# Optimization experiments

Measured on AMD Instinct MI355X. Metric: run time of the kernel, lower is better.

Reference implementation:

```python
import jax, jax.numpy as jnp
import numpy as np

B, Q, C = 8, 100, 1024
H, W = 64, 64
NH = 16
HD = C // NH
SCALE = HD ** -0.5
LN_EPS = 1e-5


def setup_inputs() -> dict:
    key = jax.random.key(0)
    ks = jax.random.split(key, 8)
    xav = lambda k, shp: jax.random.normal(k, shp, jnp.float32) * (2.0 / (shp[0] + shp[-1])) ** 0.5
    return {
        "tgt": jax.random.normal(ks[0], (B, Q, C), jnp.float32),
        "memory": jax.random.normal(ks[1], (B, H, W, C), jnp.float32),
        "memory_pos_emb": jax.random.normal(ks[2], (B, H, W, C), jnp.float32),
        "query_pos_emb": jax.random.normal(ks[3], (B, Q, C), jnp.float32),
        "Wq": xav(ks[4], (C, C)),
        "Wk": xav(ks[5], (C, C)),
        "Wv": xav(ks[6], (C, C)),
        "Wo": xav(ks[7], (C, C)),
        "bo": jnp.zeros((C,), jnp.float32),
        "ln_gamma": jnp.ones((C,), jnp.float32),
        "ln_beta": jnp.zeros((C,), jnp.float32),
    }


def _layernorm(x, g, b):
    mu = jnp.mean(x, axis=-1, keepdims=True)
    var = jnp.var(x, axis=-1, keepdims=True)
    return (x - mu) * jax.lax.rsqrt(var + LN_EPS) * g + b


def reference(tgt, memory, memory_pos_emb, query_pos_emb, Wq, Wk, Wv, Wo, bo, ln_gamma, ln_beta):
    # flatten spatial dims: [B,H,W,C] -> [B,K,C]
    mem = memory.reshape(B, H * W, C)
    mpos = memory_pos_emb.reshape(B, H * W, C)
    q_in = tgt + query_pos_emb          # [B,Q,C]
    k_in = mem + mpos                    # [B,K,C]
    # projections (torch Linear: x @ W.T), split heads -> [B,nh,*,hd]
    q = (q_in @ Wq.T).reshape(B, Q, NH, HD).transpose(0, 2, 1, 3)
    k = (k_in @ Wk.T).reshape(B, -1, NH, HD).transpose(0, 2, 1, 3)
    v = (mem @ Wv.T).reshape(B, -1, NH, HD).transpose(0, 2, 1, 3)
    dots = jnp.einsum('bhid,bhjd->bhij', q, k) * SCALE   # [B,nh,Q,K]
    # slot attention: softmax over QUERY axis, then renormalize over keys
    attn = jax.nn.softmax(dots, axis=2)
    attn = attn / (jnp.sum(attn, axis=-1, keepdims=True) + 1e-8)
    updates = jnp.einsum('bhij,bhjd->bhid', attn, v)     # [B,nh,Q,hd]
    updates = updates.transpose(0, 2, 1, 3).reshape(B, Q, C)
    out = updates @ Wo.T + bo
    # residual (dropout is identity in eval) + post-LayerNorm
    return _layernorm(tgt + out, ln_gamma, ln_beta)
```

## Files before the change

kernel.cpp:

```cpp
#include <hip/hip_runtime.h>

typedef unsigned short u16;
typedef __attribute__((ext_vector_type(8))) short bf16x8;
typedef __attribute__((ext_vector_type(4))) short bf16x4;
typedef __attribute__((ext_vector_type(4))) float f32x4;
typedef __attribute__((ext_vector_type(4))) unsigned short u16x4;
typedef __attribute__((ext_vector_type(4))) int i32x4;
typedef __attribute__((ext_vector_type(4))) float f4;

#define DI __device__ __forceinline__


DI u16 f2bf(float f){
  unsigned int u = __float_as_uint(f);
  return (u16)((u + 0x7FFFu + ((u >> 16) & 1u)) >> 16);
}

DI void gl_lds16(const void* g, void* l){
  __builtin_amdgcn_global_load_lds((const __attribute__((address_space(1))) unsigned int*)g,
                                   (__attribute__((address_space(3))) unsigned int*)l, 16, 0, 0);
}

__global__ __launch_bounds__(256) void prep_kv(const float* __restrict__ mem,
                                               const float* __restrict__ mpos,
                                               u16* __restrict__ kA, u16* __restrict__ vA){
  size_t gid = (size_t)blockIdx.x * 256 + threadIdx.x;
  f4 m = ((const f4*)mem)[gid];
  f4 p = ((const f4*)mpos)[gid];
  u16x4 k, v;
  #pragma unroll
  for (int j = 0; j < 4; ++j){ k[j] = f2bf(m[j] + p[j]); v[j] = f2bf(m[j]); }
  ((u16x4*)kA)[gid] = k;
  ((u16x4*)vA)[gid] = v;
}

__global__ __launch_bounds__(256) void prep_qw(const float* __restrict__ tgt,
                                               const float* __restrict__ qpos,
                                               const float* __restrict__ Wq, const float* __restrict__ Wk,
                                               const float* __restrict__ Wv, const float* __restrict__ Wo,
                                               u16* __restrict__ qA, u16* __restrict__ Wbf){
  int gid = blockIdx.x * 256 + threadIdx.x;
  const int NQ4 = 819200 / 4;
  if (gid < NQ4){
    f4 a = ((const f4*)tgt)[gid];
    f4 b = ((const f4*)qpos)[gid];
    u16x4 r;
    #pragma unroll
    for (int j = 0; j < 4; ++j) r[j] = f2bf(a[j] + b[j]);
    ((u16x4*)qA)[gid] = r;
  } else {
    int wid = gid - NQ4;
    int sel = wid >> 18;
    int off = wid & 262143;
    const float* W = (sel == 0) ? Wq : (sel == 1) ? Wk : (sel == 2) ? Wv : Wo;
    f4 w = ((const f4*)W)[off];
    u16x4 r;
    #pragma unroll
    for (int j = 0; j < 4; ++j) r[j] = f2bf(w[j]);
    ((u16x4*)(Wbf))[(size_t)sel * 262144 + off] = r;
  }
}

template<int MODE>
__global__ __launch_bounds__(256, 2) void gemm_bt(
    const u16* __restrict__ A, const u16* __restrict__ Bw,
    u16* __restrict__ Cb, float* __restrict__ Cf,
    const float* __restrict__ bias, const float* __restrict__ resid,
    int M, float scale)
{
  __shared__ u16 lA[2][128 * 32];
  __shared__ u16 lB[2][128 * 32];
  const int tid = threadIdx.x;
  const int l = tid & 63, w = tid >> 6;
  const int nwg = gridDim.x;
  int bid = blockIdx.x;
  bid = (bid & 7) * (nwg >> 3) + (bid >> 3);
  const int mb = bid >> 3, nb = bid & 7;
  const int m0 = mb * 128, n0 = nb * 128;
  const int fr = l & 15, fg = l >> 4;
  const int wr = w >> 1, wc = w & 1;

  f32x4 acc[4][4] = {};

  auto stage = [&](int buf, int kt){
    const int k0 = kt * 32;
    #pragma unroll
    for (int q = 0; q < 2; ++q){
      int r = w * 32 + q * 16 + (l >> 2);
      int ar = m0 + r; if (ar >= M) ar = M - 1;
      gl_lds16(A  + (size_t)ar * 1024 + k0 + (l & 3) * 8, &lA[buf][(w * 32 + q * 16) * 32]);
      gl_lds16(Bw + (size_t)(n0 + r) * 1024 + k0 + (l & 3) * 8, &lB[buf][(w * 32 + q * 16) * 32]);
    }
  };

  stage(0, 0);
  __syncthreads();
  for (int kt = 0; kt < 32; ++kt){
    const int cur = kt & 1;
    if (kt < 31) stage(cur ^ 1, kt + 1);
    bf16x8 av[4], bv[4];
    #pragma unroll
    for (int m = 0; m < 4; ++m)
      av[m] = *(const bf16x8*)&lA[cur][(wr * 64 + m * 16 + fr) * 32 + fg * 8];
    #pragma unroll
    for (int n = 0; n < 4; ++n)
      bv[n] = *(const bf16x8*)&lB[cur][(wc * 64 + n * 16 + fr) * 32 + fg * 8];
    #pragma unroll
    for (int m = 0; m < 4; ++m)
      #pragma unroll
      for (int n = 0; n < 4; ++n)
        acc[m][n] = __builtin_amdgcn_mfma_f32_16x16x32_bf16(av[m], bv[n], acc[m][n], 0, 0, 0);
    __syncthreads();
  }

  #pragma unroll
  for (int m = 0; m < 4; ++m){
    const int grow_base = m0 + wr * 64 + m * 16 + fg * 4;
    #pragma unroll
    for (int n = 0; n < 4; ++n){
      const int gcol = n0 + wc * 64 + n * 16 + fr;
      #pragma unroll
      for (int r = 0; r < 4; ++r){
        const int grow = grow_base + r;
        if (grow < M){
          const float v = acc[m][n][r];
          if (MODE == 0) Cb[(size_t)grow * 1024 + gcol] = f2bf(v * scale);
          else           Cf[(size_t)grow * 1024 + gcol] = v + bias[gcol] + resid[(size_t)grow * 1024 + gcol];
        }
      }
    }
  }
}

__global__ __launch_bounds__(64, 1) void attn_k(
    const u16* __restrict__ qp, const u16* __restrict__ kp, const u16* __restrict__ vp,
    float* __restrict__ updpart, float* __restrict__ rspart)
{
  const int bidx = blockIdx.x;
  const int c = bidx & 7, h = (bidx >> 3) & 15, b = bidx >> 7;
  const int bh = b * 16 + h;
  const int l = threadIdx.x;
  const int fr = l & 15, fg = l >> 4;

  __shared__ u16 qlds[112 * 64];
  for (int t = 0; t < 14; ++t){
    int chunk = t * 64 + l;
    int row = chunk >> 3, cb = chunk & 7;
    i32x4 val = {0, 0, 0, 0};
    if (row < 100)
      val = *(const i32x4*)(qp + (size_t)(b * 100 + row) * 1024 + h * 64 + cb * 8);
    *(i32x4*)((char*)qlds + row * 128 + ((cb ^ (row & 7)) * 16)) = val;
  }
  __syncthreads();

  bf16x8 qf[7][2];
  #pragma unroll
  for (int n = 0; n < 7; ++n)
    #pragma unroll
    for (int ks = 0; ks < 2; ++ks){
      int row = n * 16 + fr;
      int cb = ks * 4 + fg;
      qf[n][ks] = *(const bf16x8*)((const char*)qlds + row * 128 + ((cb ^ (row & 7)) * 16));
    }

  f32x4 acc[7][4] = {};
  float rs[7] = {};
  const f32x4 fz = {0.f, 0.f, 0.f, 0.f};
  const size_t kvbase = ((size_t)b * 4096) * 1024 + h * 64;

  for (int t = 0; t < 32; ++t){
    const int j0 = c * 512 + t * 16;
    bf16x8 kf0 = *(const bf16x8*)(kp + kvbase + (size_t)(j0 + fr) * 1024 + fg * 8);
    bf16x8 kf1 = *(const bf16x8*)(kp + kvbase + (size_t)(j0 + fr) * 1024 + 32 + fg * 8);
    f32x4 s[7];
    #pragma unroll
    for (int n = 0; n < 7; ++n){
      s[n] = __builtin_amdgcn_mfma_f32_16x16x32_bf16(kf0, qf[n][0], fz, 0, 0, 0);
      s[n] = __builtin_amdgcn_mfma_f32_16x16x32_bf16(kf1, qf[n][1], s[n], 0, 0, 0);
    }
    if (fr >= 4){ s[6][0] = -1e30f; s[6][1] = -1e30f; s[6][2] = -1e30f; s[6][3] = -1e30f; }

    float pv[7][4];
    #pragma unroll
    for (int r = 0; r < 4; ++r){
      float m = s[0][r];
      #pragma unroll
      for (int n = 1; n < 7; ++n) m = fmaxf(m, s[n][r]);
      m = fmaxf(m, __shfl_xor(m, 1)); m = fmaxf(m, __shfl_xor(m, 2));
      m = fmaxf(m, __shfl_xor(m, 4)); m = fmaxf(m, __shfl_xor(m, 8));
      float sum = 0.f;
      #pragma unroll
      for (int n = 0; n < 7; ++n){ float e = __expf(s[n][r] - m); pv[n][r] = e; sum += e; }
      sum += __shfl_xor(sum, 1); sum += __shfl_xor(sum, 2);
      sum += __shfl_xor(sum, 4); sum += __shfl_xor(sum, 8);
      float inv = 1.0f / sum;
      #pragma unroll
      for (int n = 0; n < 7; ++n) pv[n][r] *= inv;
    }

    bf16x4 pk[7];
    #pragma unroll
    for (int n = 0; n < 7; ++n){
      rs[n] += pv[n][0] + pv[n][1] + pv[n][2] + pv[n][3];
      bf16x4 t4;
      t4[0] = (short)f2bf(pv[n][0]); t4[1] = (short)f2bf(pv[n][1]);
      t4[2] = (short)f2bf(pv[n][2]); t4[3] = (short)f2bf(pv[n][3]);
      pk[n] = t4;
    }

    bf16x4 vf[4];
    #pragma unroll
    for (int dt = 0; dt < 4; ++dt){
      bf16x4 tv;
      #pragma unroll
      for (int jj = 0; jj < 4; ++jj)
        tv[jj] = (short)vp[kvbase + (size_t)(j0 + fg * 4 + jj) * 1024 + dt * 16 + fr];
      vf[dt] = tv;
    }

    #pragma unroll
    for (int n = 0; n < 7; ++n)
      #pragma unroll
      for (int dt = 0; dt < 4; ++dt)
        acc[n][dt] = __builtin_amdgcn_mfma_f32_16x16x16bf16_1k(vf[dt], pk[n], acc[n][dt], 0, 0, 0);
  }

  #pragma unroll
  for (int n = 0; n < 7; ++n){
    float v = rs[n];
    v += __shfl_xor(v, 16); v += __shfl_xor(v, 32);
    if (l < 16) rspart[((size_t)c * 128 + bh) * 112 + n * 16 + l] = v;
  }
  float* ub = updpart + ((size_t)c * 128 + bh) * 64 * 112;
  #pragma unroll
  for (int n = 0; n < 7; ++n)
    #pragma unroll
    for (int dt = 0; dt < 4; ++dt)
      #pragma unroll
      for (int r = 0; r < 4; ++r){
        int d = dt * 16 + fg * 4 + r;
        int i = n * 16 + fr;
        ub[d * 112 + i] = acc[n][dt][r];
      }
}

__global__ __launch_bounds__(256) void nrm_k(const float* __restrict__ updpart,
                                             const float* __restrict__ rspart,
                                             u16* __restrict__ updn){
  int gid = blockIdx.x * 256 + threadIdx.x;
  int b = gid / 102400;
  int rem = gid % 102400;
  int i = rem / 1024;
  int cc = rem & 1023;
  int h = cc >> 6, d = cc & 63;
  int bh = b * 16 + h;
  float sum = 0.f, rsum = 0.f;
  #pragma unroll
  for (int c = 0; c < 8; ++c){
    sum  += updpart[(((size_t)c * 128 + bh) * 64 + d) * 112 + i];
    rsum += rspart[((size_t)c * 128 + bh) * 112 + i];
  }
  updn[gid] = f2bf(sum / (rsum + 1e-8f));
}

__global__ __launch_bounds__(256) void ln_k(const float* __restrict__ x,
                                            const float* __restrict__ g,
                                            const float* __restrict__ be,
                                            float* __restrict__ out){
  const int row = blockIdx.x;
  const int tid = threadIdx.x;
  const f4 xv = *(const f4*)(x + (size_t)row * 1024 + tid * 4);
  float s = xv[0] + xv[1] + xv[2] + xv[3];
  float q = xv[0]*xv[0] + xv[1]*xv[1] + xv[2]*xv[2] + xv[3]*xv[3];
  #pragma unroll
  for (int m = 1; m < 64; m <<= 1){ s += __shfl_xor(s, m); q += __shfl_xor(q, m); }
  __shared__ float ss[4], qq[4];
  const int w = tid >> 6;
  if ((tid & 63) == 0){ ss[w] = s; qq[w] = q; }
  __syncthreads();
  s = ss[0] + ss[1] + ss[2] + ss[3];
  q = qq[0] + qq[1] + qq[2] + qq[3];
  const float mu = s * (1.0f / 1024.0f);
  const float var = q * (1.0f / 1024.0f) - mu * mu;
  const float rstd = rsqrtf(var + 1e-5f);
  const f4 gv = *(const f4*)(g + tid * 4);
  const f4 bv = *(const f4*)(be + tid * 4);
  f4 o;
  #pragma unroll
  for (int j = 0; j < 4; ++j) o[j] = (xv[j] - mu) * rstd * gv[j] + bv[j];
  *(f4*)(out + (size_t)row * 1024 + tid * 4) = o;
}

extern "C" void kernel_launch(void* const* d_in, const int* in_sizes, int n_in,
                              void* d_out, int out_size, void* d_ws, size_t ws_size,
                              hipStream_t stream)
{
  const float* tgt   = (const float*)d_in[0];
  const float* mem   = (const float*)d_in[1];
  const float* mpos  = (const float*)d_in[2];
  const float* qpos  = (const float*)d_in[3];
  const float* Wq    = (const float*)d_in[4];
  const float* Wk    = (const float*)d_in[5];
  const float* Wv    = (const float*)d_in[6];
  const float* Wo    = (const float*)d_in[7];
  const float* bo    = (const float*)d_in[8];
  const float* gamma = (const float*)d_in[9];
  const float* beta  = (const float*)d_in[10];

  char* ws = (char*)d_ws;
  u16* qA     = (u16*)(ws + 0);
  u16* Wbf    = (u16*)(ws + 1638400);
  u16* kA     = (u16*)(ws + 10027008);
  u16* vA     = (u16*)(ws + 77135872);
  u16* qproj  = (u16*)(ws + 144244736);
  u16* kproj  = (u16*)(ws + 145883136);
  u16* vproj  = kA;
  float* updpart = (float*)(ws + 77135872);
  float* rspart  = (float*)(ws + 77135872 + 29360128);
  u16*   updn    = (u16*)  (ws + 77135872 + 29818880);
  float* resid   = (float*)(ws + 77135872 + 31457280);

  prep_kv<<<32768, 256, 0, stream>>>(mem, mpos, kA, vA);
  prep_qw<<<4896, 256, 0, stream>>>(tgt, qpos, Wq, Wk, Wv, Wo, qA, Wbf);
  gemm_bt<0><<<56,   256, 0, stream>>>(qA, Wbf,            qproj, nullptr, nullptr, nullptr, 800,   0.125f);
  gemm_bt<0><<<2048, 256, 0, stream>>>(kA, Wbf + 1048576,  kproj, nullptr, nullptr, nullptr, 32768, 1.0f);
  gemm_bt<0><<<2048, 256, 0, stream>>>(vA, Wbf + 2097152,  vproj, nullptr, nullptr, nullptr, 32768, 1.0f);
  attn_k<<<1024, 64, 0, stream>>>(qproj, kproj, vproj, updpart, rspart);
  nrm_k<<<3200, 256, 0, stream>>>(updpart, rspart, updn);
  gemm_bt<1><<<56, 256, 0, stream>>>(updn, Wbf + 3145728, nullptr, resid, bo, tgt, 800, 1.0f);
  ln_k<<<800, 256, 0, stream>>>(resid, gamma, beta, (float*)d_out);
}
```

Measured before the change: 415.8 us.

## Add 256x256-tile 8-wave GEMM for K/V projections and batch prep_kv loads

Adds a new gemm256 kernel with 256x256 output tiles, 512 threads, double-buffered LDS staging through global_load_lds, XOR-swizzled LDS reads, and interleaved barriers with setprio around MFMA groups. The large K and V projections now use it in place of the 128-tile gemm_bt, which should raise data reuse per tile and overlap loads with MFMA. Separately, prep_kv now has each thread handle four strided vectors so more loads are in flight per thread. The bigger tile brings high register pressure (128 accumulator floats per thread) and only one block per CU.

```diff
diff --git a/kernel.cpp b/kernel.cpp
--- a/kernel.cpp
+++ b/kernel.cpp
@@ -24,14 +24,24 @@
 __global__ __launch_bounds__(256) void prep_kv(const float* __restrict__ mem,
                                                const float* __restrict__ mpos,
                                                u16* __restrict__ kA, u16* __restrict__ vA){
-  size_t gid = (size_t)blockIdx.x * 256 + threadIdx.x;
-  f4 m = ((const f4*)mem)[gid];
-  f4 p = ((const f4*)mpos)[gid];
-  u16x4 k, v;
-  #pragma unroll
-  for (int j = 0; j < 4; ++j){ k[j] = f2bf(m[j] + p[j]); v[j] = f2bf(m[j]); }
-  ((u16x4*)kA)[gid] = k;
-  ((u16x4*)vA)[gid] = v;
+  const int t = blockIdx.x * 256 + threadIdx.x;
+  const int S = 2097152;
+  f4 m[4], p[4];
+  #pragma unroll
+  for (int i = 0; i < 4; ++i){
+    size_t gid = (size_t)t + (size_t)i * S;
+    m[i] = ((const f4*)mem)[gid];
+    p[i] = ((const f4*)mpos)[gid];
+  }
+  #pragma unroll
+  for (int i = 0; i < 4; ++i){
+    size_t gid = (size_t)t + (size_t)i * S;
+    u16x4 k, v;
+    #pragma unroll
+    for (int j = 0; j < 4; ++j){ k[j] = f2bf(m[i][j] + p[i][j]); v[j] = f2bf(m[i][j]); }
+    ((u16x4*)kA)[gid] = k;
+    ((u16x4*)vA)[gid] = v;
+  }
 }
 
 __global__ __launch_bounds__(256) void prep_qw(const float* __restrict__ tgt,
@@ -58,6 +68,127 @@
     #pragma unroll
     for (int j = 0; j < 4; ++j) r[j] = f2bf(w[j]);
     ((u16x4*)(Wbf))[(size_t)sel * 262144 + off] = r;
+  }
+}
+
+__global__ __launch_bounds__(512, 1) void gemm256(
+    const u16* __restrict__ A, const u16* __restrict__ Bw,
+    u16* __restrict__ Cb, float scale)
+{
+  __shared__ __align__(16) char lds[2][2][2][16384];
+  const int tid = threadIdx.x;
+  const int l = tid & 63, w = tid >> 6;
+  const int nwg = gridDim.x;
+  const int sbid = (blockIdx.x & 7) * (nwg >> 3) + (blockIdx.x >> 3);
+  const int mb = sbid >> 2, nb = sbid & 3;
+  const int m0 = mb * 256, n0 = nb * 256;
+  const int fr = l & 15, fg = l >> 4;
+  const int wm = w >> 2, wn = w & 3;
+
+  const int src_c2 = (l & 3) ^ ((l >> 2) & 3) ^ ((l >> 4) & 3);
+  const int rc16 = ((fg ^ ((fr & 3) ^ ((fr >> 2) & 3))) * 16);
+
+  auto stageAB = [&](int buf, int kt, int kh){
+    #pragma unroll
+    for (int q = 0; q < 2; ++q){
+      const int rr = (q * 8 + w) * 16 + (l >> 2);
+      const size_t gofs = (size_t)kt * 64 + (size_t)kh * 32 + (size_t)src_c2 * 8;
+      gl_lds16(A  + (size_t)(m0 + rr) * 1024 + gofs, &lds[buf][0][kh][(q * 8 + w) * 1024]);
+      gl_lds16(Bw + (size_t)(n0 + rr) * 1024 + gofs, &lds[buf][1][kh][(q * 8 + w) * 1024]);
+    }
+  };
+
+  f32x4 acc[8][4] = {};
+
+  stageAB(0, 0, 0);
+  stageAB(0, 0, 1);
+  stageAB(1, 1, 0);
+  asm volatile("s_waitcnt vmcnt(8)" ::: "memory");
+  __builtin_amdgcn_s_barrier();
+  __builtin_amdgcn_sched_barrier(0);
+
+  for (int kt = 0; kt < 16; ++kt){
+    const int p = kt & 1;
+    const int kt1 = (kt + 1 > 15) ? 15 : kt + 1;
+    const int kt2 = (kt + 2 > 15) ? 15 : kt + 2;
+    bf16x8 av[8], b0, b1, b2, b3;
+
+    #pragma unroll
+    for (int mf = 0; mf < 8; ++mf)
+      av[mf] = *(const bf16x8*)(&lds[p][0][0][0] + (wm * 128 + mf * 16 + fr) * 64 + rc16);
+    b0 = *(const bf16x8*)(&lds[p][1][0][0] + (wn * 64 +  0 + fr) * 64 + rc16);
+    b1 = *(const bf16x8*)(&lds[p][1][0][0] + (wn * 64 + 16 + fr) * 64 + rc16);
+    stageAB(p ^ 1, kt1, 1);
+    __builtin_amdgcn_s_barrier(); __builtin_amdgcn_sched_barrier(0);
+    __builtin_amdgcn_s_setprio(1);
+    #pragma unroll
+    for (int mf = 0; mf < 8; ++mf){
+      acc[mf][0] = __builtin_amdgcn_mfma_f32_16x16x32_bf16(av[mf], b0, acc[mf][0], 0, 0, 0);
+      acc[mf][1] = __builtin_amdgcn_mfma_f32_16x16x32_bf16(av[mf], b1, acc[mf][1], 0, 0, 0);
+    }
+    __builtin_amdgcn_s_setprio(0);
+    __builtin_amdgcn_sched_barrier(0);
+    __builtin_amdgcn_s_barrier(); __builtin_amdgcn_sched_barrier(0);
+
+    b2 = *(const bf16x8*)(&lds[p][1][0][0] + (wn * 64 + 32 + fr) * 64 + rc16);
+    b3 = *(const bf16x8*)(&lds[p][1][0][0] + (wn * 64 + 48 + fr) * 64 + rc16);
+    asm volatile("s_waitcnt vmcnt(8)" ::: "memory");
+    __builtin_amdgcn_s_barrier(); __builtin_amdgcn_sched_barrier(0);
+    __builtin_amdgcn_s_setprio(1);
+    #pragma unroll
+    for (int mf = 0; mf < 8; ++mf){
+      acc[mf][2] = __builtin_amdgcn_mfma_f32_16x16x32_bf16(av[mf], b2, acc[mf][2], 0, 0, 0);
+      acc[mf][3] = __builtin_amdgcn_mfma_f32_16x16x32_bf16(av[mf], b3, acc[mf][3], 0, 0, 0);
+    }
+    __builtin_amdgcn_s_setprio(0);
+    __builtin_amdgcn_sched_barrier(0);
+    __builtin_amdgcn_s_barrier(); __builtin_amdgcn_sched_barrier(0);
+
+    #pragma unroll
+    for (int mf = 0; mf < 8; ++mf)
+      av[mf] = *(const bf16x8*)(&lds[p][0][1][0] + (wm * 128 + mf * 16 + fr) * 64 + rc16);
+    b0 = *(const bf16x8*)(&lds[p][1][1][0] + (wn * 64 +  0 + fr) * 64 + rc16);
+    b1 = *(const bf16x8*)(&lds[p][1][1][0] + (wn * 64 + 16 + fr) * 64 + rc16);
+    stageAB(p, kt2, 0);
+    __builtin_amdgcn_s_barrier(); __builtin_amdgcn_sched_barrier(0);
+    __builtin_amdgcn_s_setprio(1);
+    #pragma unroll
+    for (int mf = 0; mf < 8; ++mf){
+      acc[mf][0] = __builtin_amdgcn_mfma_f32_16x16x32_bf16(av[mf], b0, acc[mf][0], 0, 0, 0);
+      acc[mf][1] = __builtin_amdgcn_mfma_f32_16x16x32_bf16(av[mf], b1, acc[mf][1], 0, 0, 0);
+    }
+    __builtin_amdgcn_s_setprio(0);
+    __builtin_amdgcn_sched_barrier(0);
+    __builtin_amdgcn_s_barrier(); __builtin_amdgcn_sched_barrier(0);
+
+    b2 = *(const bf16x8*)(&lds[p][1][1][0] + (wn * 64 + 32 + fr) * 64 + rc16);
+    b3 = *(const bf16x8*)(&lds[p][1][1][0] + (wn * 64 + 48 + fr) * 64 + rc16);
+    asm volatile("s_waitcnt vmcnt(8)" ::: "memory");
+    __builtin_amdgcn_s_barrier(); __builtin_amdgcn_sched_barrier(0);
+    __builtin_amdgcn_s_setprio(1);
+    #pragma unroll
+    for (int mf = 0; mf < 8; ++mf){
+      acc[mf][2] = __builtin_amdgcn_mfma_f32_16x16x32_bf16(av[mf], b2, acc[mf][2], 0, 0, 0);
+      acc[mf][3] = __builtin_amdgcn_mfma_f32_16x16x32_bf16(av[mf], b3, acc[mf][3], 0, 0, 0);
+    }
+    __builtin_amdgcn_s_setprio(0);
+    __builtin_amdgcn_sched_barrier(0);
+    __builtin_amdgcn_s_barrier(); __builtin_amdgcn_sched_barrier(0);
+  }
+
+  asm volatile("s_waitcnt vmcnt(0)" ::: "memory");
+
+  #pragma unroll
+  for (int mf = 0; mf < 8; ++mf){
+    #pragma unroll
+    for (int nf = 0; nf < 4; ++nf){
+      const int gcol = n0 + wn * 64 + nf * 16 + fr;
+      #pragma unroll
+      for (int r = 0; r < 4; ++r){
+        const int grow = m0 + wm * 128 + mf * 16 + fg * 4 + r;
+        Cb[(size_t)grow * 1024 + gcol] = f2bf(acc[mf][nf][r] * scale);
+      }
+    }
   }
 }
 
@@ -320,11 +451,11 @@
   u16*   updn    = (u16*)  (ws + 77135872 + 29818880);
   float* resid   = (float*)(ws + 77135872 + 31457280);
 
-  prep_kv<<<32768, 256, 0, stream>>>(mem, mpos, kA, vA);
+  prep_kv<<<8192, 256, 0, stream>>>(mem, mpos, kA, vA);
   prep_qw<<<4896, 256, 0, stream>>>(tgt, qpos, Wq, Wk, Wv, Wo, qA, Wbf);
-  gemm_bt<0><<<56,   256, 0, stream>>>(qA, Wbf,            qproj, nullptr, nullptr, nullptr, 800,   0.125f);
-  gemm_bt<0><<<2048, 256, 0, stream>>>(kA, Wbf + 1048576,  kproj, nullptr, nullptr, nullptr, 32768, 1.0f);
-  gemm_bt<0><<<2048, 256, 0, stream>>>(vA, Wbf + 2097152,  vproj, nullptr, nullptr, nullptr, 32768, 1.0f);
+  gemm_bt<0><<<56,  256, 0, stream>>>(qA, Wbf, qproj, nullptr, nullptr, nullptr, 800, 0.125f);
+  gemm256<<<512, 512, 0, stream>>>(kA, Wbf + 1048576, kproj, 1.0f);
+  gemm256<<<512, 512, 0, stream>>>(vA, Wbf + 2097152, vproj, 1.0f);
   attn_k<<<1024, 64, 0, stream>>>(qproj, kproj, vproj, updpart, rspart);
   nrm_k<<<3200, 256, 0, stream>>>(updpart, rspart, updn);
   gemm_bt<1><<<56, 256, 0, stream>>>(updn, Wbf + 3145728, nullptr, resid, bo, tgt, 800, 1.0f);
```

Result: faster. 392.8 us (-5.5%).
